# Kernel tuning notes

Hardware: AMD Instinct MI355X
Metric: run time of the kernel (lower is better)

Reference implementation:

```python
import jax, jax.numpy as jnp
import numpy as np
from jax.ops import segment_sum

N_PFAS, N_GW, N_SW = 50000, 200000, 20000
D_IN, D_OUT, D_EDGE = 32, 32, 3
E_PG, E_GP, E_PS, E_SP = 2000000, 2000000, 1000000, 1000000


def _params(key):
    ks = jax.random.split(key, 24)
    g = lambda k, s: jax.random.normal(k, s, dtype=jnp.float32) * 0.05
    p = {}
    # SAGEConvWithEdgeAttr for pg (pfas->gw) and gp (gw->pfas)
    for i, rel in enumerate(['pg', 'gp']):
        o = i * 5
        p[f'Wl_{rel}'] = g(ks[o + 0], (D_IN, D_OUT))
        p[f'bl_{rel}'] = g(ks[o + 1], (D_OUT,))
        p[f'Wr_{rel}'] = g(ks[o + 2], (D_IN, D_OUT))
        p[f'We_{rel}'] = g(ks[o + 3], (D_EDGE, D_OUT))
        p[f'be_{rel}'] = g(ks[o + 4], (D_OUT,))
    # plain SAGEConv for ps (pfas->sw) and sp (sw->pfas)
    for i, rel in enumerate(['ps', 'sp']):
        o = 10 + i * 3
        p[f'Wl_{rel}'] = g(ks[o + 0], (D_IN, D_OUT))
        p[f'bl_{rel}'] = g(ks[o + 1], (D_OUT,))
        p[f'Wr_{rel}'] = g(ks[o + 2], (D_IN, D_OUT))
    p['W_out'] = g(ks[16], (D_OUT, 1))
    p['b_out'] = g(ks[17], (1,))
    p['a_prelu'] = jnp.float32(0.25) * jnp.ones((1,), jnp.float32)
    return p


def setup_inputs() -> dict:
    key = jax.random.key(0)
    ks = jax.random.split(key, 16)
    inp = {
        'x_pfas': jax.random.normal(ks[0], (N_PFAS, D_IN), jnp.float32),
        'x_gw': jax.random.normal(ks[1], (N_GW, D_IN), jnp.float32),
        'x_sw': jax.random.normal(ks[2], (N_SW, D_IN), jnp.float32),
        'src_pg': jax.random.randint(ks[3], (E_PG,), 0, N_PFAS),
        'dst_pg': jax.random.randint(ks[4], (E_PG,), 0, N_GW),
        'ea_pg': jax.random.uniform(ks[5], (E_PG, D_EDGE), jnp.float32),
        'src_gp': jax.random.randint(ks[6], (E_GP,), 0, N_GW),
        'dst_gp': jax.random.randint(ks[7], (E_GP,), 0, N_PFAS),
        'ea_gp': jax.random.uniform(ks[8], (E_GP, D_EDGE), jnp.float32),
        'src_ps': jax.random.randint(ks[9], (E_PS,), 0, N_PFAS),
        'dst_ps': jax.random.randint(ks[10], (E_PS,), 0, N_SW),
        'src_sp': jax.random.randint(ks[11], (E_SP,), 0, N_SW),
        'dst_sp': jax.random.randint(ks[12], (E_SP,), 0, N_PFAS),
    }
    inp.update(_params(ks[13]))
    return inp


def _sage(x_src, x_dst, src, dst, Wl, bl, Wr, n_dst):
    # PyG SAGEConv: lin_l(mean_aggr(x_j)) + lin_r(x_dst); lin_r has no bias
    msg = x_src[src]                                   # [E, D_IN]
    s = segment_sum(msg, dst, num_segments=n_dst)      # [n_dst, D_IN]
    cnt = segment_sum(jnp.ones((src.shape[0],), x_src.dtype), dst, num_segments=n_dst)
    mean = s / jnp.maximum(cnt, 1.0)[:, None]
    return mean @ Wl + bl + x_dst @ Wr


def _edge_scatter_set(dst, ea_t, n_dst):
    # matches torch zeros.scatter_(0, col, edge_attr_transformed): overwrite at dst
    return jnp.zeros((n_dst, ea_t.shape[1]), ea_t.dtype).at[dst].set(ea_t)


def reference(x_pfas, x_gw, x_sw,
              src_pg, dst_pg, ea_pg,
              src_gp, dst_gp, ea_gp,
              src_ps, dst_ps, src_sp, dst_sp,
              Wl_pg, bl_pg, Wr_pg, We_pg, be_pg,
              Wl_gp, bl_gp, Wr_gp, We_gp, be_gp,
              Wl_ps, bl_ps, Wr_ps,
              Wl_sp, bl_sp, Wr_sp,
              W_out, b_out, a_prelu):
    # pfas -> gw (edge attrs)
    out_gw = _sage(x_pfas, x_gw, src_pg, dst_pg, Wl_pg, bl_pg, Wr_pg, N_GW)
    out_gw = out_gw + _edge_scatter_set(dst_pg, ea_pg @ We_pg + be_pg, N_GW)
    # gw -> pfas (edge attrs)
    out_pf1 = _sage(x_gw, x_pfas, src_gp, dst_gp, Wl_gp, bl_gp, Wr_gp, N_PFAS)
    out_pf1 = out_pf1 + _edge_scatter_set(dst_gp, ea_gp @ We_gp + be_gp, N_PFAS)
    # sw -> pfas (plain SAGE)
    out_pf2 = _sage(x_sw, x_pfas, src_sp, dst_sp, Wl_sp, bl_sp, Wr_sp, N_PFAS)
    # pfas -> sw (plain SAGE)
    out_sw = _sage(x_pfas, x_sw, src_ps, dst_ps, Wl_ps, bl_ps, Wr_ps, N_SW)
    # HeteroConv aggr='sum' over relations with same dst type, then relu
    h_pfas = jax.nn.relu(out_pf1 + out_pf2)
    h_gw = jax.nn.relu(out_gw)
    h_sw = jax.nn.relu(out_sw)
    # final linear + PReLU on gw_wells
    y = h_gw @ W_out + b_out                           # [N_GW, 1]
    y = jnp.where(y >= 0, y, a_prelu * y)
    return h_pfas, y, h_sw
```

## Files before the change

### kernel.cpp

```cpp
#include <hip/hip_runtime.h>
#include <hip/hip_fp16.h>

typedef unsigned int u32;
typedef unsigned long long u64;

#define NPFAS 50000
#define NGW   200000
#define NSW   20000
#define D     32
#define EPG   2000000
#define EGP   2000000
#define EPS   1000000
#define ESP   1000000

#define NB_PG 782
#define NB_GP 782
#define NB_SP 391
#define NB_PS 313
#define CAP_PG 2880
#define CAP_GP 2880
#define CAP_SP 2880
#define CAP_PS 3584
#define SORT_MAX 3584

#define ZGCUR    0
#define MAXE_PG  2304
#define MAXE_GP  202304
#define S_PG     252304
#define S_GP     6652304
#define S_SP     8252304
#define S_PS     9852304
#define CNT_PG   10492304
#define CNT_GP   10692304
#define CNT_SP   10742304
#define CNT_PS   10792304
#define REG_PG   10812304
#define REG_GP   15316624
#define REG_SP   19820944
#define REG_PS   20947024
#define XH_PFAS  22068816
#define XH_GW    22868816

__global__ __launch_bounds__(256) void convert_x(
    const float* __restrict__ xp, const float* __restrict__ xg, int* __restrict__ wsi)
{
    int i = blockIdx.x * 256 + threadIdx.x;
    __half2* hp = (__half2*)(wsi + XH_PFAS);
    __half2* hg = (__half2*)(wsi + XH_GW);
    const float2* fp = (const float2*)xp;
    const float2* fg = (const float2*)xg;
    if (i < NPFAS * D / 2) {
        float2 v = fp[i];
        hp[i] = __floats2half2_rn(v.x, v.y);
        return;
    }
    i -= NPFAS * D / 2;
    if (i < NGW * D / 2) {
        float2 v = fg[i];
        hg[i] = __floats2half2_rn(v.x, v.y);
    }
}

__device__ __forceinline__ void part4_narrow(
    const int* __restrict__ src, const int* __restrict__ dst,
    int e0, int e1, int nb, int cp, int cf, int pshift, int bbits, int roundSz,
    u32* __restrict__ region, int cap, int* __restrict__ gcur,
    u32* binData, u32* binCnt)
{
    u32 dlm = (1u << bbits) - 1u;
    for (int b = threadIdx.x; b < nb; b += 256) binCnt[b] = 0;
    __syncthreads();
    for (int base = e0; base < e1; base += roundSz) {
        int rend = base + roundSz; if (rend > e1) rend = e1;
        for (int e = base + (int)threadIdx.x; e < rend; e += 256) {
            int d = dst[e];
            int bk = d >> bbits;
            u32 w0 = (u32)src[e] | (((u32)d & dlm) << pshift);
            u32 pos = atomicAdd(&binCnt[bk], 1u);
            if ((int)pos < cp) {
                binData[bk * cp + (int)pos] = w0;
            } else {
                int g = atomicAdd(&gcur[bk], 1);
                if (g < cap) region[(size_t)bk * cap + g] = w0;
            }
        }
        __syncthreads();
        bool last = (base + roundSz >= e1);
        for (int b = threadIdx.x; b < nb; b += 256) {
            int c = (int)binCnt[b];
            if (c > cp) c = cp;
            if (c >= cf || (last && c > 0)) {
                int g = atomicAdd(&gcur[b], c);
                int lim = cap - g; if (lim < 0) lim = 0; if (c > lim) c = lim;
                u32* dp = region + ((size_t)b * cap + g);
                for (int i = 0; i < c; i++) dp[i] = binData[b * cp + i];
                binCnt[b] = 0;
            }
        }
        __syncthreads();
    }
}

__device__ __forceinline__ void part4_wide(
    const int* __restrict__ src, const int* __restrict__ dst,
    int e0, int e1, int nb, int cp, int cf, int bbits, int roundSz,
    u64* __restrict__ region, int cap, int* __restrict__ gcur,
    u64* binData, u32* binCnt)
{
    u32 dlm = (1u << bbits) - 1u;
    for (int b = threadIdx.x; b < nb; b += 256) binCnt[b] = 0;
    __syncthreads();
    for (int base = e0; base < e1; base += roundSz) {
        int rend = base + roundSz; if (rend > e1) rend = e1;
        for (int e = base + (int)threadIdx.x; e < rend; e += 256) {
            int d = dst[e];
            int bk = d >> bbits;
            u64 w0 = ((u64)(u32)e << 32) | (u32)src[e] | (((u32)d & dlm) << 21);
            u32 pos = atomicAdd(&binCnt[bk], 1u);
            if ((int)pos < cp) {
                binData[bk * cp + (int)pos] = w0;
            } else {
                int g = atomicAdd(&gcur[bk], 1);
                if (g < cap) region[(size_t)bk * cap + g] = w0;
            }
        }
        __syncthreads();
        bool last = (base + roundSz >= e1);
        for (int b = threadIdx.x; b < nb; b += 256) {
            int c = (int)binCnt[b];
            if (c > cp) c = cp;
            if (c >= cf || (last && c > 0)) {
                int g = atomicAdd(&gcur[b], c);
                int lim = cap - g; if (lim < 0) lim = 0; if (c > lim) c = lim;
                u64* dp = region + ((size_t)b * cap + g);
                for (int i = 0; i < c; i++) dp[i] = binData[b * cp + i];
                binCnt[b] = 0;
            }
        }
        __syncthreads();
    }
}

__global__ __launch_bounds__(256) void partition_all(
    const int* __restrict__ src_pg, const int* __restrict__ dst_pg,
    const int* __restrict__ src_gp, const int* __restrict__ dst_gp,
    const int* __restrict__ src_sp, const int* __restrict__ dst_sp,
    const int* __restrict__ src_ps, const int* __restrict__ dst_ps,
    int* __restrict__ wsi)
{
    __shared__ __align__(16) u64 binData64[6256];
    __shared__ u32 binCnt[782];
    u32* ws = (u32*)wsi;
    int b = blockIdx.x;
    if (b < 160) {
        int e0 = b * (EPG / 160);
        part4_wide(src_pg, dst_pg, e0, e0 + EPG / 160, NB_PG, 8, 6, 8, 1024,
                   (u64*)(ws + REG_PG), CAP_PG, wsi + ZGCUR + 0, binData64, binCnt);
    } else if (b < 320) {
        int bb = b - 160;
        int e0 = bb * (EGP / 160);
        part4_wide(src_gp, dst_gp, e0, e0 + EGP / 160, NB_GP, 8, 6, 6, 1024,
                   (u64*)(ws + REG_GP), CAP_GP, wsi + ZGCUR + 782, binData64, binCnt);
    } else if (b < 416) {
        int bb = b - 320;
        int e0 = (int)(((long long)bb * ESP) / 96);
        int e1 = (int)(((long long)(bb + 1) * ESP) / 96);
        part4_narrow(src_sp, dst_sp, e0, e1, NB_SP, 32, 24, 15, 7, 1024,
                     ws + REG_SP, CAP_SP, wsi + ZGCUR + 1564, (u32*)binData64, binCnt);
    } else {
        int bb = b - 416;
        int e0 = (int)(((long long)bb * EPS) / 96);
        int e1 = (int)(((long long)(bb + 1) * EPS) / 96);
        part4_narrow(src_ps, dst_ps, e0, e1, NB_PS, 32, 24, 16, 6, 1024,
                     ws + REG_PS, CAP_PS, wsi + ZGCUR + 1955, (u32*)binData64, binCnt);
    }
}

__global__ __launch_bounds__(256) void sort_agg(
    const float* __restrict__ x_sw,
    int* __restrict__ wsi)
{
    __shared__ u32 sortedS[SORT_MAX];
    __shared__ int histS[256];
    __shared__ int startS[256];
    __shared__ int cursorS[256];
    __shared__ int mxS[256];
    __shared__ int wsum[4];

    float* wsf = (float*)wsi;
    u32* wsu = (u32*)wsi;
    int tid = threadIdx.x;
    int bid = blockIdx.x;

    const __half* xh = nullptr; const float* xf = nullptr;
    const u64* reg64 = nullptr; const u32* reg32 = nullptr;
    int gi, cap, pshift, nbDst, dbase, ndst;
    u32 smask; bool wide; float* sOut; float* cntOut; int* mxOut = nullptr;

    if (bid < NB_PG) {
        xh = (const __half*)(wsi + XH_PFAS);
        reg64 = (const u64*)(wsu + REG_PG) + (size_t)bid * CAP_PG; gi = ZGCUR + bid;
        cap = CAP_PG; pshift = 21; smask = 0x1FFFFFu; wide = true;
        nbDst = 256; dbase = bid << 8; ndst = NGW;
        sOut = wsf + S_PG; cntOut = wsf + CNT_PG; mxOut = wsi + MAXE_PG;
    } else if (bid < NB_PG + NB_GP) {
        int b = bid - NB_PG;
        xh = (const __half*)(wsi + XH_GW);
        reg64 = (const u64*)(wsu + REG_GP) + (size_t)b * CAP_GP; gi = ZGCUR + 782 + b;
        cap = CAP_GP; pshift = 21; smask = 0x1FFFFFu; wide = true;
        nbDst = 64; dbase = b << 6; ndst = NPFAS;
        sOut = wsf + S_GP; cntOut = wsf + CNT_GP; mxOut = wsi + MAXE_GP;
    } else if (bid < NB_PG + NB_GP + NB_SP) {
        int b = bid - NB_PG - NB_GP;
        xf = x_sw;
        reg32 = wsu + REG_SP + (size_t)b * CAP_SP; gi = ZGCUR + 1564 + b;
        cap = CAP_SP; pshift = 15; smask = 0x7FFFu; wide = false;
        nbDst = 128; dbase = b << 7; ndst = NPFAS;
        sOut = wsf + S_SP; cntOut = wsf + CNT_SP;
    } else {
        int b = bid - NB_PG - NB_GP - NB_SP;
        xh = (const __half*)(wsi + XH_PFAS);
        reg32 = wsu + REG_PS + (size_t)b * CAP_PS; gi = ZGCUR + 1955 + b;
        cap = CAP_PS; pshift = 16; smask = 0xFFFFu; wide = false;
        nbDst = 64; dbase = b << 6; ndst = NSW;
        sOut = wsf + S_PS; cntOut = wsf + CNT_PS;
    }

    int nEnt = wsi[gi]; if (nEnt > cap) nEnt = cap;

    histS[tid] = 0;
    mxS[tid] = -1;
    __syncthreads();

    if (wide) {
        for (int i = tid; i < nEnt; i += 256) {
            u64 w = reg64[i];
            int dl = (int)(((u32)w >> 21) & 255u);
            atomicAdd(&histS[dl], 1);
            atomicMax(&mxS[dl], (int)(u32)(w >> 32));
        }
    } else {
        for (int i = tid; i < nEnt; i += 256) {
            u32 w = reg32[i];
            int dl = (int)((w >> pshift) & 255u);
            atomicAdd(&histS[dl], 1);
        }
    }
    __syncthreads();

    {
        int v = histS[tid];
        int lane = tid & 63, w = tid >> 6;
        int incl = v;
#pragma unroll
        for (int off = 1; off < 64; off <<= 1) {
            int t = __shfl_up(incl, off);
            if (lane >= off) incl += t;
        }
        if (lane == 63) wsum[w] = incl;
        startS[tid] = incl - v;
    }
    __syncthreads();
    {
        int w = tid >> 6;
        int off = 0;
        for (int k = 0; k < w; k++) off += wsum[k];
        int st = startS[tid] + off;
        startS[tid] = st;
        cursorS[tid] = st;
    }
    __syncthreads();

    if (wide) {
        for (int i = tid; i < nEnt; i += 256) {
            u64 w = reg64[i];
            int dl = (int)(((u32)w >> 21) & 255u);
            int pos = atomicAdd(&cursorS[dl], 1);
            if (pos < SORT_MAX) sortedS[pos] = (u32)w & smask;
        }
    } else {
        for (int i = tid; i < nEnt; i += 256) {
            u32 w = reg32[i];
            int dl = (int)((w >> pshift) & 255u);
            int pos = atomicAdd(&cursorS[dl], 1);
            if (pos < SORT_MAX) sortedS[pos] = w & smask;
        }
    }
    __syncthreads();

    int wv = tid >> 6, lane = tid & 63, half = lane >> 5, f = lane & 31;
    for (int q = wv; q < nbDst; q += 4) {
        int dn = dbase + q;
        if (dn >= ndst) continue;
        int deg = histS[q];
        int p0 = startS[q];
        float a = 0.f;
        int i = half;
        if (xh) {
            for (; i + 6 < deg; i += 8) {
                int s0 = (int)sortedS[p0 + i];
                int s1 = (int)sortedS[p0 + i + 2];
                int s2 = (int)sortedS[p0 + i + 4];
                int s3 = (int)sortedS[p0 + i + 6];
                float v0 = __half2float(xh[(size_t)s0 * D + f]);
                float v1 = __half2float(xh[(size_t)s1 * D + f]);
                float v2 = __half2float(xh[(size_t)s2 * D + f]);
                float v3 = __half2float(xh[(size_t)s3 * D + f]);
                a += (v0 + v1) + (v2 + v3);
            }
            for (; i < deg; i += 2) a += __half2float(xh[(size_t)sortedS[p0 + i] * D + f]);
        } else {
            for (; i + 6 < deg; i += 8) {
                int s0 = (int)sortedS[p0 + i];
                int s1 = (int)sortedS[p0 + i + 2];
                int s2 = (int)sortedS[p0 + i + 4];
                int s3 = (int)sortedS[p0 + i + 6];
                float v0 = xf[(size_t)s0 * D + f];
                float v1 = xf[(size_t)s1 * D + f];
                float v2 = xf[(size_t)s2 * D + f];
                float v3 = xf[(size_t)s3 * D + f];
                a += (v0 + v1) + (v2 + v3);
            }
            for (; i < deg; i += 2) a += xf[(size_t)sortedS[p0 + i] * D + f];
        }
        a += __shfl_xor(a, 32);
        if (half == 0) sOut[(size_t)dn * D + f] = a;
        if (lane == 0) {
            cntOut[dn] = (float)deg;
            if (wide) mxOut[dn] = mxS[q];
        }
    }
}

__global__ __launch_bounds__(256) void finalize_gw(
    const float* __restrict__ s, const float* __restrict__ cntF,
    const int* __restrict__ maxe,
    const float* __restrict__ x_gw,
    const float* __restrict__ ea,
    const float* __restrict__ Wl, const float* __restrict__ bl,
    const float* __restrict__ Wr, const float* __restrict__ We,
    const float* __restrict__ be,
    const float* __restrict__ W_out, const float* __restrict__ b_out,
    const float* __restrict__ a_prelu,
    float* __restrict__ y_out)
{
    __shared__ __align__(16) float WlT[D * D];
    __shared__ __align__(16) float WrT[D * D];
    __shared__ float WeT[3 * D];
    __shared__ float blS[D], beS[D], WoS[D];
    for (int i = threadIdx.x; i < D * D; i += blockDim.x) {
        int k = i / D, j = i % D;
        WlT[j * D + k] = Wl[i];
        WrT[j * D + k] = Wr[i];
    }
    for (int i = threadIdx.x; i < 3 * D; i += blockDim.x) {
        int k = i / D, j = i % D;
        WeT[j * 3 + k] = We[i];
    }
    if (threadIdx.x < D) {
        blS[threadIdx.x] = bl[threadIdx.x];
        beS[threadIdx.x] = be[threadIdx.x];
        WoS[threadIdx.x] = W_out[threadIdx.x];
    }
    __syncthreads();

    int n = blockIdx.x * blockDim.x + threadIdx.x;
    if (n >= NGW) return;

    float mean[D], xd[D];
    float inv = 1.0f / fmaxf(cntF[n], 1.0f);
    const float4* sp = (const float4*)(s + (size_t)n * D);
    const float4* xp = (const float4*)(x_gw + (size_t)n * D);
#pragma unroll
    for (int q = 0; q < D / 4; q++) {
        float4 sv = sp[q];
        mean[4*q+0] = sv.x * inv; mean[4*q+1] = sv.y * inv;
        mean[4*q+2] = sv.z * inv; mean[4*q+3] = sv.w * inv;
        float4 xv = xp[q];
        xd[4*q+0] = xv.x; xd[4*q+1] = xv.y; xd[4*q+2] = xv.z; xd[4*q+3] = xv.w;
    }
    int me = maxe[n];
    bool he = (me >= 0);
    float e0 = 0.f, e1 = 0.f, e2 = 0.f;
    if (he) {
        e0 = ea[(size_t)me * 3 + 0];
        e1 = ea[(size_t)me * 3 + 1];
        e2 = ea[(size_t)me * 3 + 2];
    }
    float yacc = 0.f;
    for (int j = 0; j < D; j++) {
        float o = blS[j] + (he ? beS[j] : 0.0f);
        const float4* wl4 = (const float4*)(WlT + j * D);
        const float4* wr4 = (const float4*)(WrT + j * D);
#pragma unroll
        for (int q = 0; q < D / 4; q++) {
            float4 wl = wl4[q], wr = wr4[q];
            o += mean[4*q+0]*wl.x + mean[4*q+1]*wl.y + mean[4*q+2]*wl.z + mean[4*q+3]*wl.w;
            o += xd[4*q+0]*wr.x + xd[4*q+1]*wr.y + xd[4*q+2]*wr.z + xd[4*q+3]*wr.w;
        }
        if (he) o += e0*WeT[j*3+0] + e1*WeT[j*3+1] + e2*WeT[j*3+2];
        float h = fmaxf(o, 0.0f);
        yacc += h * WoS[j];
    }
    float y = yacc + b_out[0];
    float ap = a_prelu[0];
    y_out[n] = (y >= 0.f) ? y : ap * y;
}

__global__ __launch_bounds__(256) void finalize_pfas(
    const float* __restrict__ s_gp, const float* __restrict__ cnt_gp,
    const int* __restrict__ maxe_gp,
    const float* __restrict__ s_sp, const float* __restrict__ cnt_sp,
    const float* __restrict__ x_pfas,
    const float* __restrict__ ea,
    const float* __restrict__ Wl_gp, const float* __restrict__ bl_gp,
    const float* __restrict__ Wr_gp, const float* __restrict__ We_gp,
    const float* __restrict__ be_gp,
    const float* __restrict__ Wl_sp, const float* __restrict__ bl_sp,
    const float* __restrict__ Wr_sp,
    float* __restrict__ h_out)
{
    __shared__ __align__(16) float WlgT[D * D];
    __shared__ __align__(16) float WlsT[D * D];
    __shared__ __align__(16) float WrcT[D * D];
    __shared__ float WeT[3 * D];
    __shared__ float blc[D], beS[D];
    for (int i = threadIdx.x; i < D * D; i += blockDim.x) {
        int k = i / D, j = i % D;
        WlgT[j * D + k] = Wl_gp[i];
        WlsT[j * D + k] = Wl_sp[i];
        WrcT[j * D + k] = Wr_gp[i] + Wr_sp[i];
    }
    for (int i = threadIdx.x; i < 3 * D; i += blockDim.x) {
        int k = i / D, j = i % D;
        WeT[j * 3 + k] = We_gp[i];
    }
    if (threadIdx.x < D) {
        blc[threadIdx.x] = bl_gp[threadIdx.x] + bl_sp[threadIdx.x];
        beS[threadIdx.x] = be_gp[threadIdx.x];
    }
    __syncthreads();

    int n = blockIdx.x * blockDim.x + threadIdx.x;
    if (n >= NPFAS) return;

    float mg[D], ms[D], xd[D];
    float invg = 1.0f / fmaxf(cnt_gp[n], 1.0f);
    float invs = 1.0f / fmaxf(cnt_sp[n], 1.0f);
    const float4* gp4 = (const float4*)(s_gp + (size_t)n * D);
    const float4* sp4 = (const float4*)(s_sp + (size_t)n * D);
    const float4* xp4 = (const float4*)(x_pfas + (size_t)n * D);
#pragma unroll
    for (int q = 0; q < D / 4; q++) {
        float4 a = gp4[q];
        mg[4*q+0] = a.x * invg; mg[4*q+1] = a.y * invg; mg[4*q+2] = a.z * invg; mg[4*q+3] = a.w * invg;
        float4 b = sp4[q];
        ms[4*q+0] = b.x * invs; ms[4*q+1] = b.y * invs; ms[4*q+2] = b.z * invs; ms[4*q+3] = b.w * invs;
        float4 c = xp4[q];
        xd[4*q+0] = c.x; xd[4*q+1] = c.y; xd[4*q+2] = c.z; xd[4*q+3] = c.w;
    }
    int me = maxe_gp[n];
    bool he = (me >= 0);
    float e0 = 0.f, e1 = 0.f, e2 = 0.f;
    if (he) {
        e0 = ea[(size_t)me * 3 + 0];
        e1 = ea[(size_t)me * 3 + 1];
        e2 = ea[(size_t)me * 3 + 2];
    }
    float* out = h_out + (size_t)n * D;
    for (int j = 0; j < D; j++) {
        float o = blc[j] + (he ? beS[j] : 0.0f);
        const float4* wg4 = (const float4*)(WlgT + j * D);
        const float4* ws4 = (const float4*)(WlsT + j * D);
        const float4* wc4 = (const float4*)(WrcT + j * D);
#pragma unroll
        for (int q = 0; q < D / 4; q++) {
            float4 wg = wg4[q], wsv = ws4[q], wc = wc4[q];
            o += mg[4*q+0]*wg.x + mg[4*q+1]*wg.y + mg[4*q+2]*wg.z + mg[4*q+3]*wg.w;
            o += ms[4*q+0]*wsv.x + ms[4*q+1]*wsv.y + ms[4*q+2]*wsv.z + ms[4*q+3]*wsv.w;
            o += xd[4*q+0]*wc.x + xd[4*q+1]*wc.y + xd[4*q+2]*wc.z + xd[4*q+3]*wc.w;
        }
        if (he) o += e0*WeT[j*3+0] + e1*WeT[j*3+1] + e2*WeT[j*3+2];
        out[j] = fmaxf(o, 0.0f);
    }
}

__global__ __launch_bounds__(256) void finalize_sw(
    const float* __restrict__ s, const float* __restrict__ cntF,
    const float* __restrict__ x_sw,
    const float* __restrict__ Wl, const float* __restrict__ bl,
    const float* __restrict__ Wr,
    float* __restrict__ h_out)
{
    __shared__ __align__(16) float WlT[D * D];
    __shared__ __align__(16) float WrT[D * D];
    __shared__ float blS[D];
    for (int i = threadIdx.x; i < D * D; i += blockDim.x) {
        int k = i / D, j = i % D;
        WlT[j * D + k] = Wl[i];
        WrT[j * D + k] = Wr[i];
    }
    if (threadIdx.x < D) blS[threadIdx.x] = bl[threadIdx.x];
    __syncthreads();

    int n = blockIdx.x * blockDim.x + threadIdx.x;
    if (n >= NSW) return;

    float mean[D], xd[D];
    float inv = 1.0f / fmaxf(cntF[n], 1.0f);
    const float4* sp = (const float4*)(s + (size_t)n * D);
    const float4* xp = (const float4*)(x_sw + (size_t)n * D);
#pragma unroll
    for (int q = 0; q < D / 4; q++) {
        float4 sv = sp[q];
        mean[4*q+0] = sv.x * inv; mean[4*q+1] = sv.y * inv;
        mean[4*q+2] = sv.z * inv; mean[4*q+3] = sv.w * inv;
        float4 xv = xp[q];
        xd[4*q+0] = xv.x; xd[4*q+1] = xv.y; xd[4*q+2] = xv.z; xd[4*q+3] = xv.w;
    }
    float* out = h_out + (size_t)n * D;
    for (int j = 0; j < D; j++) {
        float o = blS[j];
        const float4* wl4 = (const float4*)(WlT + j * D);
        const float4* wr4 = (const float4*)(WrT + j * D);
#pragma unroll
        for (int q = 0; q < D / 4; q++) {
            float4 wl = wl4[q], wr = wr4[q];
            o += mean[4*q+0]*wl.x + mean[4*q+1]*wl.y + mean[4*q+2]*wl.z + mean[4*q+3]*wl.w;
            o += xd[4*q+0]*wr.x + xd[4*q+1]*wr.y + xd[4*q+2]*wr.z + xd[4*q+3]*wr.w;
        }
        out[j] = fmaxf(o, 0.0f);
    }
}

extern "C" void kernel_launch(void* const* d_in, const int* in_sizes, int n_in,
                              void* d_out, int out_size, void* d_ws, size_t ws_size,
                              hipStream_t stream) {
    (void)in_sizes; (void)n_in; (void)out_size; (void)ws_size;
    const float* x_pfas = (const float*)d_in[0];
    const float* x_gw   = (const float*)d_in[1];
    const float* x_sw   = (const float*)d_in[2];
    const int*   src_pg = (const int*)d_in[3];
    const int*   dst_pg = (const int*)d_in[4];
    const float* ea_pg  = (const float*)d_in[5];
    const int*   src_gp = (const int*)d_in[6];
    const int*   dst_gp = (const int*)d_in[7];
    const float* ea_gp  = (const float*)d_in[8];
    const int*   src_ps = (const int*)d_in[9];
    const int*   dst_ps = (const int*)d_in[10];
    const int*   src_sp = (const int*)d_in[11];
    const int*   dst_sp = (const int*)d_in[12];
    const float* Wl_pg = (const float*)d_in[13];
    const float* bl_pg = (const float*)d_in[14];
    const float* Wr_pg = (const float*)d_in[15];
    const float* We_pg = (const float*)d_in[16];
    const float* be_pg = (const float*)d_in[17];
    const float* Wl_gp = (const float*)d_in[18];
    const float* bl_gp = (const float*)d_in[19];
    const float* Wr_gp = (const float*)d_in[20];
    const float* We_gp = (const float*)d_in[21];
    const float* be_gp = (const float*)d_in[22];
    const float* Wl_ps = (const float*)d_in[23];
    const float* bl_ps = (const float*)d_in[24];
    const float* Wr_ps = (const float*)d_in[25];
    const float* Wl_sp = (const float*)d_in[26];
    const float* bl_sp = (const float*)d_in[27];
    const float* Wr_sp = (const float*)d_in[28];
    const float* W_out = (const float*)d_in[29];
    const float* b_out = (const float*)d_in[30];
    const float* a_pre = (const float*)d_in[31];

    int*   wsi = (int*)d_ws;
    float* wsf = (float*)d_ws;

    hipMemsetAsync(wsi + ZGCUR, 0, 2304 * sizeof(int), stream);

    convert_x<<<(NPFAS * D / 2 + NGW * D / 2 + 255) / 256, 256, 0, stream>>>(
        x_pfas, x_gw, wsi);

    partition_all<<<512, 256, 0, stream>>>(src_pg, dst_pg, src_gp, dst_gp,
                                           src_sp, dst_sp, src_ps, dst_ps, wsi);

    sort_agg<<<NB_PG + NB_GP + NB_SP + NB_PS, 256, 0, stream>>>(x_sw, wsi);

    float* out    = (float*)d_out;
    float* h_pfas = out;
    float* y_out  = out + 1600000;
    float* h_sw   = out + 1800000;

    finalize_pfas<<<(NPFAS + 255) / 256, 256, 0, stream>>>(
        wsf + S_GP, wsf + CNT_GP, wsi + MAXE_GP, wsf + S_SP, wsf + CNT_SP,
        x_pfas, ea_gp,
        Wl_gp, bl_gp, Wr_gp, We_gp, be_gp,
        Wl_sp, bl_sp, Wr_sp, h_pfas);

    finalize_gw<<<(NGW + 255) / 256, 256, 0, stream>>>(
        wsf + S_PG, wsf + CNT_PG, wsi + MAXE_PG, x_gw, ea_pg,
        Wl_pg, bl_pg, Wr_pg, We_pg, be_pg,
        W_out, b_out, a_pre, y_out);

    finalize_sw<<<(NSW + 255) / 256, 256, 0, stream>>>(
        wsf + S_PS, wsf + CNT_PS, x_sw, Wl_ps, bl_ps, Wr_ps, h_sw);
}
```

Before: 485.9 us.

## Fuse conversion into partition, vectorize gather, merge finalize kernels

Folds the fp32-to-fp16 feature conversion into extra blocks of the partition kernel, so it runs alongside edge binning instead of as a separate launch. Doubles the partition round size, which flushes bins less often. Rewrites the sort_agg gather so each lane loads a half2/float2 pair, with four rows per wave, to widen loads. Merges the three finalize kernels into one launch, trading fewer launches and tail effects for a larger shared-memory footprint and more branching per block.

```diff
diff --git a/kernel.cpp b/kernel.cpp
--- a/kernel.cpp
+++ b/kernel.cpp
@@ -41,25 +41,8 @@
 #define XH_PFAS  22068816
 #define XH_GW    22868816
 
-__global__ __launch_bounds__(256) void convert_x(
-    const float* __restrict__ xp, const float* __restrict__ xg, int* __restrict__ wsi)
-{
-    int i = blockIdx.x * 256 + threadIdx.x;
-    __half2* hp = (__half2*)(wsi + XH_PFAS);
-    __half2* hg = (__half2*)(wsi + XH_GW);
-    const float2* fp = (const float2*)xp;
-    const float2* fg = (const float2*)xg;
-    if (i < NPFAS * D / 2) {
-        float2 v = fp[i];
-        hp[i] = __floats2half2_rn(v.x, v.y);
-        return;
-    }
-    i -= NPFAS * D / 2;
-    if (i < NGW * D / 2) {
-        float2 v = fg[i];
-        hg[i] = __floats2half2_rn(v.x, v.y);
-    }
-}
+#define PART_BLOCKS 512
+#define CONV_BLOCKS 256
 
 __device__ __forceinline__ void part4_narrow(
     const int* __restrict__ src, const int* __restrict__ dst,
@@ -141,37 +124,57 @@
     }
 }
 
-__global__ __launch_bounds__(256) void partition_all(
+__global__ __launch_bounds__(256) void partition_conv(
     const int* __restrict__ src_pg, const int* __restrict__ dst_pg,
     const int* __restrict__ src_gp, const int* __restrict__ dst_gp,
     const int* __restrict__ src_sp, const int* __restrict__ dst_sp,
     const int* __restrict__ src_ps, const int* __restrict__ dst_ps,
+    const float* __restrict__ x_pfas, const float* __restrict__ x_gw,
     int* __restrict__ wsi)
 {
     __shared__ __align__(16) u64 binData64[6256];
     __shared__ u32 binCnt[782];
     u32* ws = (u32*)wsi;
     int b = blockIdx.x;
+    if (b >= PART_BLOCKS) {
+        __half2* hp = (__half2*)(wsi + XH_PFAS);
+        __half2* hg = (__half2*)(wsi + XH_GW);
+        const float2* fp = (const float2*)x_pfas;
+        const float2* fg = (const float2*)x_gw;
+        int idx = (b - PART_BLOCKS) * 256 + (int)threadIdx.x;
+        const int NTP = NPFAS * D / 2;
+        const int NTT = NTP + NGW * D / 2;
+        for (int i = idx; i < NTT; i += CONV_BLOCKS * 256) {
+            if (i < NTP) {
+                float2 v = fp[i];
+                hp[i] = __floats2half2_rn(v.x, v.y);
+            } else {
+                float2 v = fg[i - NTP];
+                hg[i - NTP] = __floats2half2_rn(v.x, v.y);
+            }
+        }
+        return;
+    }
     if (b < 160) {
         int e0 = b * (EPG / 160);
-        part4_wide(src_pg, dst_pg, e0, e0 + EPG / 160, NB_PG, 8, 6, 8, 1024,
+        part4_wide(src_pg, dst_pg, e0, e0 + EPG / 160, NB_PG, 8, 6, 8, 2048,
                    (u64*)(ws + REG_PG), CAP_PG, wsi + ZGCUR + 0, binData64, binCnt);
     } else if (b < 320) {
         int bb = b - 160;
         int e0 = bb * (EGP / 160);
-        part4_wide(src_gp, dst_gp, e0, e0 + EGP / 160, NB_GP, 8, 6, 6, 1024,
+        part4_wide(src_gp, dst_gp, e0, e0 + EGP / 160, NB_GP, 8, 6, 6, 2048,
                    (u64*)(ws + REG_GP), CAP_GP, wsi + ZGCUR + 782, binData64, binCnt);
     } else if (b < 416) {
         int bb = b - 320;
         int e0 = (int)(((long long)bb * ESP) / 96);
         int e1 = (int)(((long long)(bb + 1) * ESP) / 96);
-        part4_narrow(src_sp, dst_sp, e0, e1, NB_SP, 32, 24, 15, 7, 1024,
+        part4_narrow(src_sp, dst_sp, e0, e1, NB_SP, 32, 24, 15, 7, 2048,
                      ws + REG_SP, CAP_SP, wsi + ZGCUR + 1564, (u32*)binData64, binCnt);
     } else {
         int bb = b - 416;
         int e0 = (int)(((long long)bb * EPS) / 96);
         int e1 = (int)(((long long)(bb + 1) * EPS) / 96);
-        part4_narrow(src_ps, dst_ps, e0, e1, NB_PS, 32, 24, 16, 6, 1024,
+        part4_narrow(src_ps, dst_ps, e0, e1, NB_PS, 32, 24, 16, 6, 2048,
                      ws + REG_PS, CAP_PS, wsi + ZGCUR + 1955, (u32*)binData64, binCnt);
     }
 }
@@ -192,34 +195,34 @@
     int tid = threadIdx.x;
     int bid = blockIdx.x;
 
-    const __half* xh = nullptr; const float* xf = nullptr;
+    const __half2* xh2 = nullptr; const float2* xf2 = nullptr;
     const u64* reg64 = nullptr; const u32* reg32 = nullptr;
     int gi, cap, pshift, nbDst, dbase, ndst;
     u32 smask; bool wide; float* sOut; float* cntOut; int* mxOut = nullptr;
 
     if (bid < NB_PG) {
-        xh = (const __half*)(wsi + XH_PFAS);
+        xh2 = (const __half2*)(wsi + XH_PFAS);
         reg64 = (const u64*)(wsu + REG_PG) + (size_t)bid * CAP_PG; gi = ZGCUR + bid;
         cap = CAP_PG; pshift = 21; smask = 0x1FFFFFu; wide = true;
         nbDst = 256; dbase = bid << 8; ndst = NGW;
         sOut = wsf + S_PG; cntOut = wsf + CNT_PG; mxOut = wsi + MAXE_PG;
     } else if (bid < NB_PG + NB_GP) {
         int b = bid - NB_PG;
-        xh = (const __half*)(wsi + XH_GW);
+        xh2 = (const __half2*)(wsi + XH_GW);
         reg64 = (const u64*)(wsu + REG_GP) + (size_t)b * CAP_GP; gi = ZGCUR + 782 + b;
         cap = CAP_GP; pshift = 21; smask = 0x1FFFFFu; wide = true;
         nbDst = 64; dbase = b << 6; ndst = NPFAS;
         sOut = wsf + S_GP; cntOut = wsf + CNT_GP; mxOut = wsi + MAXE_GP;
     } else if (bid < NB_PG + NB_GP + NB_SP) {
         int b = bid - NB_PG - NB_GP;
-        xf = x_sw;
+        xf2 = (const float2*)x_sw;
         reg32 = wsu + REG_SP + (size_t)b * CAP_SP; gi = ZGCUR + 1564 + b;
         cap = CAP_SP; pshift = 15; smask = 0x7FFFu; wide = false;
         nbDst = 128; dbase = b << 7; ndst = NPFAS;
         sOut = wsf + S_SP; cntOut = wsf + CNT_SP;
     } else {
         int b = bid - NB_PG - NB_GP - NB_SP;
-        xh = (const __half*)(wsi + XH_PFAS);
+        xh2 = (const __half2*)(wsi + XH_PFAS);
         reg32 = wsu + REG_PS + (size_t)b * CAP_PS; gi = ZGCUR + 1955 + b;
         cap = CAP_PS; pshift = 16; smask = 0xFFFFu; wide = false;
         nbDst = 64; dbase = b << 6; ndst = NSW;
@@ -288,43 +291,57 @@
     }
     __syncthreads();
 
-    int wv = tid >> 6, lane = tid & 63, half = lane >> 5, f = lane & 31;
+    int wv = tid >> 6, lane = tid & 63;
+    int rs = lane >> 4;
+    int fp = lane & 15;
     for (int q = wv; q < nbDst; q += 4) {
         int dn = dbase + q;
         if (dn >= ndst) continue;
         int deg = histS[q];
         int p0 = startS[q];
-        float a = 0.f;
-        int i = half;
-        if (xh) {
-            for (; i + 6 < deg; i += 8) {
-                int s0 = (int)sortedS[p0 + i];
-                int s1 = (int)sortedS[p0 + i + 2];
-                int s2 = (int)sortedS[p0 + i + 4];
-                int s3 = (int)sortedS[p0 + i + 6];
-                float v0 = __half2float(xh[(size_t)s0 * D + f]);
-                float v1 = __half2float(xh[(size_t)s1 * D + f]);
-                float v2 = __half2float(xh[(size_t)s2 * D + f]);
-                float v3 = __half2float(xh[(size_t)s3 * D + f]);
-                a += (v0 + v1) + (v2 + v3);
-            }
-            for (; i < deg; i += 2) a += __half2float(xh[(size_t)sortedS[p0 + i] * D + f]);
+        float ax = 0.f, ay = 0.f;
+        int i = 0;
+        if (xh2) {
+            for (; i + 7 < deg; i += 8) {
+                int s0 = (int)sortedS[p0 + i + rs];
+                int s1 = (int)sortedS[p0 + i + 4 + rs];
+                __half2 h0 = xh2[s0 * 16 + fp];
+                __half2 h1 = xh2[s1 * 16 + fp];
+                float2 f0 = __half22float2(h0);
+                float2 f1 = __half22float2(h1);
+                ax += f0.x + f1.x;
+                ay += f0.y + f1.y;
+            }
+            for (; i < deg; i += 4) {
+                if (i + rs < deg) {
+                    int s0 = (int)sortedS[p0 + i + rs];
+                    float2 f0 = __half22float2(xh2[s0 * 16 + fp]);
+                    ax += f0.x; ay += f0.y;
+                }
+            }
         } else {
-            for (; i + 6 < deg; i += 8) {
-                int s0 = (int)sortedS[p0 + i];
-                int s1 = (int)sortedS[p0 + i + 2];
-                int s2 = (int)sortedS[p0 + i + 4];
-                int s3 = (int)sortedS[p0 + i + 6];
-                float v0 = xf[(size_t)s0 * D + f];
-                float v1 = xf[(size_t)s1 * D + f];
-                float v2 = xf[(size_t)s2 * D + f];
-                float v3 = xf[(size_t)s3 * D + f];
-                a += (v0 + v1) + (v2 + v3);
-            }
-            for (; i < deg; i += 2) a += xf[(size_t)sortedS[p0 + i] * D + f];
-        }
-        a += __shfl_xor(a, 32);
-        if (half == 0) sOut[(size_t)dn * D + f] = a;
+            for (; i + 7 < deg; i += 8) {
+                int s0 = (int)sortedS[p0 + i + rs];
+                int s1 = (int)sortedS[p0 + i + 4 + rs];
+                float2 f0 = xf2[s0 * 16 + fp];
+                float2 f1 = xf2[s1 * 16 + fp];
+                ax += f0.x + f1.x;
+                ay += f0.y + f1.y;
+            }
+            for (; i < deg; i += 4) {
+                if (i + rs < deg) {
+                    int s0 = (int)sortedS[p0 + i + rs];
+                    float2 f0 = xf2[s0 * 16 + fp];
+                    ax += f0.x; ay += f0.y;
+                }
+            }
+        }
+        ax += __shfl_xor(ax, 16); ay += __shfl_xor(ay, 16);
+        ax += __shfl_xor(ax, 32); ay += __shfl_xor(ay, 32);
+        if (rs == 0) {
+            float2* so2 = (float2*)(sOut + (size_t)dn * D);
+            so2[fp] = make_float2(ax, ay);
+        }
         if (lane == 0) {
             cntOut[dn] = (float)deg;
             if (wide) mxOut[dn] = mxS[q];
@@ -332,204 +349,209 @@
     }
 }
 
-__global__ __launch_bounds__(256) void finalize_gw(
-    const float* __restrict__ s, const float* __restrict__ cntF,
-    const int* __restrict__ maxe,
-    const float* __restrict__ x_gw,
-    const float* __restrict__ ea,
-    const float* __restrict__ Wl, const float* __restrict__ bl,
-    const float* __restrict__ Wr, const float* __restrict__ We,
-    const float* __restrict__ be,
+#define GW_B   782
+#define PFAS_B 196
+#define SW_B   79
+
+__global__ __launch_bounds__(256) void finalize_all(
+    const float* __restrict__ s_pg, const float* __restrict__ cnt_pg,
+    const int* __restrict__ maxe_pg, const float* __restrict__ x_gw,
+    const float* __restrict__ ea_pg,
+    const float* __restrict__ Wl_pg, const float* __restrict__ bl_pg,
+    const float* __restrict__ Wr_pg, const float* __restrict__ We_pg,
+    const float* __restrict__ be_pg,
     const float* __restrict__ W_out, const float* __restrict__ b_out,
     const float* __restrict__ a_prelu,
-    float* __restrict__ y_out)
-{
-    __shared__ __align__(16) float WlT[D * D];
-    __shared__ __align__(16) float WrT[D * D];
-    __shared__ float WeT[3 * D];
-    __shared__ float blS[D], beS[D], WoS[D];
-    for (int i = threadIdx.x; i < D * D; i += blockDim.x) {
-        int k = i / D, j = i % D;
-        WlT[j * D + k] = Wl[i];
-        WrT[j * D + k] = Wr[i];
-    }
-    for (int i = threadIdx.x; i < 3 * D; i += blockDim.x) {
-        int k = i / D, j = i % D;
-        WeT[j * 3 + k] = We[i];
-    }
-    if (threadIdx.x < D) {
-        blS[threadIdx.x] = bl[threadIdx.x];
-        beS[threadIdx.x] = be[threadIdx.x];
-        WoS[threadIdx.x] = W_out[threadIdx.x];
-    }
-    __syncthreads();
-
-    int n = blockIdx.x * blockDim.x + threadIdx.x;
-    if (n >= NGW) return;
-
-    float mean[D], xd[D];
-    float inv = 1.0f / fmaxf(cntF[n], 1.0f);
-    const float4* sp = (const float4*)(s + (size_t)n * D);
-    const float4* xp = (const float4*)(x_gw + (size_t)n * D);
-#pragma unroll
-    for (int q = 0; q < D / 4; q++) {
-        float4 sv = sp[q];
-        mean[4*q+0] = sv.x * inv; mean[4*q+1] = sv.y * inv;
-        mean[4*q+2] = sv.z * inv; mean[4*q+3] = sv.w * inv;
-        float4 xv = xp[q];
-        xd[4*q+0] = xv.x; xd[4*q+1] = xv.y; xd[4*q+2] = xv.z; xd[4*q+3] = xv.w;
-    }
-    int me = maxe[n];
-    bool he = (me >= 0);
-    float e0 = 0.f, e1 = 0.f, e2 = 0.f;
-    if (he) {
-        e0 = ea[(size_t)me * 3 + 0];
-        e1 = ea[(size_t)me * 3 + 1];
-        e2 = ea[(size_t)me * 3 + 2];
-    }
-    float yacc = 0.f;
-    for (int j = 0; j < D; j++) {
-        float o = blS[j] + (he ? beS[j] : 0.0f);
-        const float4* wl4 = (const float4*)(WlT + j * D);
-        const float4* wr4 = (const float4*)(WrT + j * D);
-#pragma unroll
-        for (int q = 0; q < D / 4; q++) {
-            float4 wl = wl4[q], wr = wr4[q];
-            o += mean[4*q+0]*wl.x + mean[4*q+1]*wl.y + mean[4*q+2]*wl.z + mean[4*q+3]*wl.w;
-            o += xd[4*q+0]*wr.x + xd[4*q+1]*wr.y + xd[4*q+2]*wr.z + xd[4*q+3]*wr.w;
-        }
-        if (he) o += e0*WeT[j*3+0] + e1*WeT[j*3+1] + e2*WeT[j*3+2];
-        float h = fmaxf(o, 0.0f);
-        yacc += h * WoS[j];
-    }
-    float y = yacc + b_out[0];
-    float ap = a_prelu[0];
-    y_out[n] = (y >= 0.f) ? y : ap * y;
-}
-
-__global__ __launch_bounds__(256) void finalize_pfas(
     const float* __restrict__ s_gp, const float* __restrict__ cnt_gp,
     const int* __restrict__ maxe_gp,
     const float* __restrict__ s_sp, const float* __restrict__ cnt_sp,
-    const float* __restrict__ x_pfas,
-    const float* __restrict__ ea,
+    const float* __restrict__ x_pfas, const float* __restrict__ ea_gp,
     const float* __restrict__ Wl_gp, const float* __restrict__ bl_gp,
     const float* __restrict__ Wr_gp, const float* __restrict__ We_gp,
     const float* __restrict__ be_gp,
     const float* __restrict__ Wl_sp, const float* __restrict__ bl_sp,
     const float* __restrict__ Wr_sp,
-    float* __restrict__ h_out)
+    const float* __restrict__ s_ps, const float* __restrict__ cnt_ps,
+    const float* __restrict__ x_sw,
+    const float* __restrict__ Wl_ps, const float* __restrict__ bl_ps,
+    const float* __restrict__ Wr_ps,
+    float* __restrict__ h_pfas, float* __restrict__ y_out, float* __restrict__ h_sw)
 {
-    __shared__ __align__(16) float WlgT[D * D];
-    __shared__ __align__(16) float WlsT[D * D];
-    __shared__ __align__(16) float WrcT[D * D];
-    __shared__ float WeT[3 * D];
-    __shared__ float blc[D], beS[D];
-    for (int i = threadIdx.x; i < D * D; i += blockDim.x) {
-        int k = i / D, j = i % D;
-        WlgT[j * D + k] = Wl_gp[i];
-        WlsT[j * D + k] = Wl_sp[i];
-        WrcT[j * D + k] = Wr_gp[i] + Wr_sp[i];
-    }
-    for (int i = threadIdx.x; i < 3 * D; i += blockDim.x) {
-        int k = i / D, j = i % D;
-        WeT[j * 3 + k] = We_gp[i];
-    }
-    if (threadIdx.x < D) {
-        blc[threadIdx.x] = bl_gp[threadIdx.x] + bl_sp[threadIdx.x];
-        beS[threadIdx.x] = be_gp[threadIdx.x];
-    }
-    __syncthreads();
-
-    int n = blockIdx.x * blockDim.x + threadIdx.x;
-    if (n >= NPFAS) return;
-
-    float mg[D], ms[D], xd[D];
-    float invg = 1.0f / fmaxf(cnt_gp[n], 1.0f);
-    float invs = 1.0f / fmaxf(cnt_sp[n], 1.0f);
-    const float4* gp4 = (const float4*)(s_gp + (size_t)n * D);
-    const float4* sp4 = (const float4*)(s_sp + (size_t)n * D);
-    const float4* xp4 = (const float4*)(x_pfas + (size_t)n * D);
-#pragma unroll
-    for (int q = 0; q < D / 4; q++) {
-        float4 a = gp4[q];
-        mg[4*q+0] = a.x * invg; mg[4*q+1] = a.y * invg; mg[4*q+2] = a.z * invg; mg[4*q+3] = a.w * invg;
-        float4 b = sp4[q];
-        ms[4*q+0] = b.x * invs; ms[4*q+1] = b.y * invs; ms[4*q+2] = b.z * invs; ms[4*q+3] = b.w * invs;
-        float4 c = xp4[q];
-        xd[4*q+0] = c.x; xd[4*q+1] = c.y; xd[4*q+2] = c.z; xd[4*q+3] = c.w;
-    }
-    int me = maxe_gp[n];
-    bool he = (me >= 0);
-    float e0 = 0.f, e1 = 0.f, e2 = 0.f;
-    if (he) {
-        e0 = ea[(size_t)me * 3 + 0];
-        e1 = ea[(size_t)me * 3 + 1];
-        e2 = ea[(size_t)me * 3 + 2];
-    }
-    float* out = h_out + (size_t)n * D;
-    for (int j = 0; j < D; j++) {
-        float o = blc[j] + (he ? beS[j] : 0.0f);
-        const float4* wg4 = (const float4*)(WlgT + j * D);
-        const float4* ws4 = (const float4*)(WlsT + j * D);
-        const float4* wc4 = (const float4*)(WrcT + j * D);
+    __shared__ __align__(16) float sh[3328];
+    int tid = threadIdx.x;
+    int b = blockIdx.x;
+
+    if (b < GW_B) {
+        float* WlT = sh;
+        float* WrT = sh + 1024;
+        float* WeT = sh + 2048;
+        float* blS = sh + 2144;
+        float* beS = sh + 2176;
+        float* WoS = sh + 2208;
+        for (int i = tid; i < D * D; i += 256) {
+            int k = i / D, j = i % D;
+            WlT[j * D + k] = Wl_pg[i];
+            WrT[j * D + k] = Wr_pg[i];
+        }
+        for (int i = tid; i < 3 * D; i += 256) {
+            int k = i / D, j = i % D;
+            WeT[j * 3 + k] = We_pg[i];
+        }
+        if (tid < D) {
+            blS[tid] = bl_pg[tid];
+            beS[tid] = be_pg[tid];
+            WoS[tid] = W_out[tid];
+        }
+        __syncthreads();
+
+        int n = b * 256 + tid;
+        if (n >= NGW) return;
+
+        float mean[D], xd[D];
+        float inv = 1.0f / fmaxf(cnt_pg[n], 1.0f);
+        const float4* sp = (const float4*)(s_pg + (size_t)n * D);
+        const float4* xp = (const float4*)(x_gw + (size_t)n * D);
 #pragma unroll
         for (int q = 0; q < D / 4; q++) {
-            float4 wg = wg4[q], wsv = ws4[q], wc = wc4[q];
-            o += mg[4*q+0]*wg.x + mg[4*q+1]*wg.y + mg[4*q+2]*wg.z + mg[4*q+3]*wg.w;
-            o += ms[4*q+0]*wsv.x + ms[4*q+1]*wsv.y + ms[4*q+2]*wsv.z + ms[4*q+3]*wsv.w;
-            o += xd[4*q+0]*wc.x + xd[4*q+1]*wc.y + xd[4*q+2]*wc.z + xd[4*q+3]*wc.w;
-        }
-        if (he) o += e0*WeT[j*3+0] + e1*WeT[j*3+1] + e2*WeT[j*3+2];
-        out[j] = fmaxf(o, 0.0f);
-    }
-}
-
-__global__ __launch_bounds__(256) void finalize_sw(
-    const float* __restrict__ s, const float* __restrict__ cntF,
-    const float* __restrict__ x_sw,
-    const float* __restrict__ Wl, const float* __restrict__ bl,
-    const float* __restrict__ Wr,
-    float* __restrict__ h_out)
-{
-    __shared__ __align__(16) float WlT[D * D];
-    __shared__ __align__(16) float WrT[D * D];
-    __shared__ float blS[D];
-    for (int i = threadIdx.x; i < D * D; i += blockDim.x) {
-        int k = i / D, j = i % D;
-        WlT[j * D + k] = Wl[i];
-        WrT[j * D + k] = Wr[i];
-    }
-    if (threadIdx.x < D) blS[threadIdx.x] = bl[threadIdx.x];
-    __syncthreads();
-
-    int n = blockIdx.x * blockDim.x + threadIdx.x;
-    if (n >= NSW) return;
-
-    float mean[D], xd[D];
-    float inv = 1.0f / fmaxf(cntF[n], 1.0f);
-    const float4* sp = (const float4*)(s + (size_t)n * D);
-    const float4* xp = (const float4*)(x_sw + (size_t)n * D);
+            float4 sv = sp[q];
+            mean[4*q+0] = sv.x * inv; mean[4*q+1] = sv.y * inv;
+            mean[4*q+2] = sv.z * inv; mean[4*q+3] = sv.w * inv;
+            float4 xv = xp[q];
+            xd[4*q+0] = xv.x; xd[4*q+1] = xv.y; xd[4*q+2] = xv.z; xd[4*q+3] = xv.w;
+        }
+        int me = maxe_pg[n];
+        bool he = (me >= 0);
+        float e0 = 0.f, e1 = 0.f, e2 = 0.f;
+        if (he) {
+            e0 = ea_pg[(size_t)me * 3 + 0];
+            e1 = ea_pg[(size_t)me * 3 + 1];
+            e2 = ea_pg[(size_t)me * 3 + 2];
+        }
+        float yacc = 0.f;
+        for (int j = 0; j < D; j++) {
+            float o = blS[j] + (he ? beS[j] : 0.0f);
+            const float4* wl4 = (const float4*)(WlT + j * D);
+            const float4* wr4 = (const float4*)(WrT + j * D);
 #pragma unroll
-    for (int q = 0; q < D / 4; q++) {
-        float4 sv = sp[q];
-        mean[4*q+0] = sv.x * inv; mean[4*q+1] = sv.y * inv;
-        mean[4*q+2] = sv.z * inv; mean[4*q+3] = sv.w * inv;
-        float4 xv = xp[q];
-        xd[4*q+0] = xv.x; xd[4*q+1] = xv.y; xd[4*q+2] = xv.z; xd[4*q+3] = xv.w;
-    }
-    float* out = h_out + (size_t)n * D;
-    for (int j = 0; j < D; j++) {
-        float o = blS[j];
-        const float4* wl4 = (const float4*)(WlT + j * D);
-        const float4* wr4 = (const float4*)(WrT + j * D);
+            for (int q = 0; q < D / 4; q++) {
+                float4 wl = wl4[q], wr = wr4[q];
+                o += mean[4*q+0]*wl.x + mean[4*q+1]*wl.y + mean[4*q+2]*wl.z + mean[4*q+3]*wl.w;
+                o += xd[4*q+0]*wr.x + xd[4*q+1]*wr.y + xd[4*q+2]*wr.z + xd[4*q+3]*wr.w;
+            }
+            if (he) o += e0*WeT[j*3+0] + e1*WeT[j*3+1] + e2*WeT[j*3+2];
+            float h = fmaxf(o, 0.0f);
+            yacc += h * WoS[j];
+        }
+        float y = yacc + b_out[0];
+        float ap = a_prelu[0];
+        y_out[n] = (y >= 0.f) ? y : ap * y;
+
+    } else if (b < GW_B + PFAS_B) {
+        float* WlgT = sh;
+        float* WlsT = sh + 1024;
+        float* WrcT = sh + 2048;
+        float* WeT  = sh + 3072;
+        float* blc  = sh + 3168;
+        float* beS  = sh + 3200;
+        for (int i = tid; i < D * D; i += 256) {
+            int k = i / D, j = i % D;
+            WlgT[j * D + k] = Wl_gp[i];
+            WlsT[j * D + k] = Wl_sp[i];
+            WrcT[j * D + k] = Wr_gp[i] + Wr_sp[i];
+        }
+        for (int i = tid; i < 3 * D; i += 256) {
+            int k = i / D, j = i % D;
+            WeT[j * 3 + k] = We_gp[i];
+        }
+        if (tid < D) {
+            blc[tid] = bl_gp[tid] + bl_sp[tid];
+            beS[tid] = be_gp[tid];
+        }
+        __syncthreads();
+
+        int n = (b - GW_B) * 256 + tid;
+        if (n >= NPFAS) return;
+
+        float mg[D], ms[D], xd[D];
+        float invg = 1.0f / fmaxf(cnt_gp[n], 1.0f);
+        float invs = 1.0f / fmaxf(cnt_sp[n], 1.0f);
+        const float4* gp4 = (const float4*)(s_gp + (size_t)n * D);
+        const float4* sp4 = (const float4*)(s_sp + (size_t)n * D);
+        const float4* xp4 = (const float4*)(x_pfas + (size_t)n * D);
 #pragma unroll
         for (int q = 0; q < D / 4; q++) {
-            float4 wl = wl4[q], wr = wr4[q];
-            o += mean[4*q+0]*wl.x + mean[4*q+1]*wl.y + mean[4*q+2]*wl.z + mean[4*q+3]*wl.w;
-            o += xd[4*q+0]*wr.x + xd[4*q+1]*wr.y + xd[4*q+2]*wr.z + xd[4*q+3]*wr.w;
-        }
-        out[j] = fmaxf(o, 0.0f);
+            float4 a = gp4[q];
+            mg[4*q+0] = a.x * invg; mg[4*q+1] = a.y * invg; mg[4*q+2] = a.z * invg; mg[4*q+3] = a.w * invg;
+            float4 bb = sp4[q];
+            ms[4*q+0] = bb.x * invs; ms[4*q+1] = bb.y * invs; ms[4*q+2] = bb.z * invs; ms[4*q+3] = bb.w * invs;
+            float4 c = xp4[q];
+            xd[4*q+0] = c.x; xd[4*q+1] = c.y; xd[4*q+2] = c.z; xd[4*q+3] = c.w;
+        }
+        int me = maxe_gp[n];
+        bool he = (me >= 0);
+        float e0 = 0.f, e1 = 0.f, e2 = 0.f;
+        if (he) {
+            e0 = ea_gp[(size_t)me * 3 + 0];
+            e1 = ea_gp[(size_t)me * 3 + 1];
+            e2 = ea_gp[(size_t)me * 3 + 2];
+        }
+        float* out = h_pfas + (size_t)n * D;
+        for (int j = 0; j < D; j++) {
+            float o = blc[j] + (he ? beS[j] : 0.0f);
+            const float4* wg4 = (const float4*)(WlgT + j * D);
+            const float4* ws4 = (const float4*)(WlsT + j * D);
+            const float4* wc4 = (const float4*)(WrcT + j * D);
+#pragma unroll
+            for (int q = 0; q < D / 4; q++) {
+                float4 wg = wg4[q], wsv = ws4[q], wc = wc4[q];
+                o += mg[4*q+0]*wg.x + mg[4*q+1]*wg.y + mg[4*q+2]*wg.z + mg[4*q+3]*wg.w;
+                o += ms[4*q+0]*wsv.x + ms[4*q+1]*wsv.y + ms[4*q+2]*wsv.z + ms[4*q+3]*wsv.w;
+                o += xd[4*q+0]*wc.x + xd[4*q+1]*wc.y + xd[4*q+2]*wc.z + xd[4*q+3]*wc.w;
+            }
+            if (he) o += e0*WeT[j*3+0] + e1*WeT[j*3+1] + e2*WeT[j*3+2];
+            out[j] = fmaxf(o, 0.0f);
+        }
+
+    } else {
+        float* WlT = sh;
+        float* WrT = sh + 1024;
+        float* blS = sh + 2048;
+        for (int i = tid; i < D * D; i += 256) {
+            int k = i / D, j = i % D;
+            WlT[j * D + k] = Wl_ps[i];
+            WrT[j * D + k] = Wr_ps[i];
+        }
+        if (tid < D) blS[tid] = bl_ps[tid];
+        __syncthreads();
+
+        int n = (b - GW_B - PFAS_B) * 256 + tid;
+        if (n >= NSW) return;
+
+        float mean[D], xd[D];
+        float inv = 1.0f / fmaxf(cnt_ps[n], 1.0f);
+        const float4* sp = (const float4*)(s_ps + (size_t)n * D);
+        const float4* xp = (const float4*)(x_sw + (size_t)n * D);
+#pragma unroll
+        for (int q = 0; q < D / 4; q++) {
+            float4 sv = sp[q];
+            mean[4*q+0] = sv.x * inv; mean[4*q+1] = sv.y * inv;
+            mean[4*q+2] = sv.z * inv; mean[4*q+3] = sv.w * inv;
+            float4 xv = xp[q];
+            xd[4*q+0] = xv.x; xd[4*q+1] = xv.y; xd[4*q+2] = xv.z; xd[4*q+3] = xv.w;
+        }
+        float* out = h_sw + (size_t)n * D;
+        for (int j = 0; j < D; j++) {
+            float o = blS[j];
+            const float4* wl4 = (const float4*)(WlT + j * D);
+            const float4* wr4 = (const float4*)(WrT + j * D);
+#pragma unroll
+            for (int q = 0; q < D / 4; q++) {
+                float4 wl = wl4[q], wr = wr4[q];
+                o += mean[4*q+0]*wl.x + mean[4*q+1]*wl.y + mean[4*q+2]*wl.z + mean[4*q+3]*wl.w;
+                o += xd[4*q+0]*wr.x + xd[4*q+1]*wr.y + xd[4*q+2]*wr.z + xd[4*q+3]*wr.w;
+            }
+            out[j] = fmaxf(o, 0.0f);
+        }
     }
 }
 
@@ -575,11 +597,10 @@
 
     hipMemsetAsync(wsi + ZGCUR, 0, 2304 * sizeof(int), stream);
 
-    convert_x<<<(NPFAS * D / 2 + NGW * D / 2 + 255) / 256, 256, 0, stream>>>(
+    partition_conv<<<PART_BLOCKS + CONV_BLOCKS, 256, 0, stream>>>(
+        src_pg, dst_pg, src_gp, dst_gp,
+        src_sp, dst_sp, src_ps, dst_ps,
         x_pfas, x_gw, wsi);
-
-    partition_all<<<512, 256, 0, stream>>>(src_pg, dst_pg, src_gp, dst_gp,
-                                           src_sp, dst_sp, src_ps, dst_ps, wsi);
 
     sort_agg<<<NB_PG + NB_GP + NB_SP + NB_PS, 256, 0, stream>>>(x_sw, wsi);
 
@@ -588,17 +609,13 @@
     float* y_out  = out + 1600000;
     float* h_sw   = out + 1800000;
 
-    finalize_pfas<<<(NPFAS + 255) / 256, 256, 0, stream>>>(
+    finalize_all<<<GW_B + PFAS_B + SW_B, 256, 0, stream>>>(
+        wsf + S_PG, wsf + CNT_PG, wsi + MAXE_PG, x_gw, ea_pg,
+        Wl_pg, bl_pg, Wr_pg, We_pg, be_pg, W_out, b_out, a_pre,
         wsf + S_GP, wsf + CNT_GP, wsi + MAXE_GP, wsf + S_SP, wsf + CNT_SP,
         x_pfas, ea_gp,
         Wl_gp, bl_gp, Wr_gp, We_gp, be_gp,
-        Wl_sp, bl_sp, Wr_sp, h_pfas);
-
-    finalize_gw<<<(NGW + 255) / 256, 256, 0, stream>>>(
-        wsf + S_PG, wsf + CNT_PG, wsi + MAXE_PG, x_gw, ea_pg,
-        Wl_pg, bl_pg, Wr_pg, We_pg, be_pg,
-        W_out, b_out, a_pre, y_out);
-
-    finalize_sw<<<(NSW + 255) / 256, 256, 0, stream>>>(
-        wsf + S_PS, wsf + CNT_PS, x_sw, Wl_ps, bl_ps, Wr_ps, h_sw);
+        Wl_sp, bl_sp, Wr_sp,
+        wsf + S_PS, wsf + CNT_PS, x_sw, Wl_ps, bl_ps, Wr_ps,
+        h_pfas, y_out, h_sw);
 }
```

Measured after the change: 436.2 us. 1.11x faster.
